# Performance work log

Hardware: AMD Instinct MI355X
Metric: run time of the kernel (lower is better)

## Reference

```python
import jax, jax.numpy as jnp
import numpy as np
from jax import lax

HD = 768; HEADS = 16; DH = HD // HEADS
KS = ((8, 8, 8), (16, 4, 4), (4, 12, 12))
ST = ((16, 32, 32), (6, 32, 32), (16, 32, 32))
T_TOK = 833; SEQ = T_TOK + 1; GH = 32


def setup_inputs() -> dict:
    key = jax.random.key(0)
    keys = iter(jax.random.split(key, 64))
    def nrm(shape, s=0.02):
        return jax.random.normal(next(keys), shape, jnp.float32) * s
    d = {}
    d["x"] = nrm((8, 3, 64, 224, 224), 1.0)
    d["spa_feas"] = nrm((8, 200, 2048), 1.0)
    d["fea_len"] = jax.random.randint(next(keys), (8,), 1, 200, dtype=jnp.int32)
    d["pos_emb"] = nrm((1, SEQ, HD), 0.02)
    d["cls_tok"] = nrm((1, 1, HD), 0.02)
    d["conv_w"] = nrm((HD, 3) + KS[0], 1.0)  # torch .normal_() std=1
    d["conv_b"] = jnp.zeros((3, HD), jnp.float32)
    d["gn_g"] = jnp.ones((HD,), jnp.float32); d["gn_b"] = jnp.zeros((HD,), jnp.float32)
    d["pin_w"] = nrm((HD, HD)); d["pin_b"] = jnp.zeros((HD,), jnp.float32)
    for nm in ("ln1", "ln2", "ln3"):
        d[nm + "_g"] = jnp.ones((HD,), jnp.float32); d[nm + "_b"] = jnp.zeros((HD,), jnp.float32)
    for nm in ("a1", "a2"):
        d[nm + "_wq"] = nrm((HD, HD)); d[nm + "_wk"] = nrm((HD, HD)); d[nm + "_wv"] = nrm((HD, HD))
        d[nm + "_wo"] = nrm((HD, HD)); d[nm + "_bo"] = jnp.zeros((HD,), jnp.float32)
    d["ff_w1"] = nrm((4 * HD, HD, 9)); d["ff_b1"] = jnp.zeros((4 * HD,), jnp.float32)
    d["ff_w2"] = nrm((HD, 4 * HD, 9)); d["ff_b2"] = jnp.zeros((HD,), jnp.float32)
    d["pout_w"] = nrm((HD, HD)); d["pout_b"] = jnp.zeros((HD,), jnp.float32)  # zero_module'd in source; random for nontrivial test
    d["spa_w"] = nrm((HD, 2048)); d["spa_b"] = jnp.zeros((HD,), jnp.float32)
    d["gru_wih"] = nrm((3 * GH, HD)); d["gru_whh"] = nrm((3 * GH, GH))
    d["gru_bih"] = jnp.zeros((3 * GH,), jnp.float32); d["gru_bhh"] = jnp.zeros((3 * GH,), jnp.float32)
    d["qh_w"] = nrm((1, GH)); d["qh_b"] = jnp.zeros((1,), jnp.float32)
    return d


def _ln(x, g, b):
    m = x.mean(-1, keepdims=True)
    v = x.var(-1, keepdims=True)
    return (x - m) / jnp.sqrt(v + 1e-5) * g + b


def _gn(x, g, b):  # x: (b, c, t), 32 groups, eps=1e-6
    bn, c, t = x.shape
    xr = x.reshape(bn, 32, c // 32, t)
    m = xr.mean((2, 3), keepdims=True)
    v = xr.var((2, 3), keepdims=True)
    xr = ((xr - m) / jnp.sqrt(v + 1e-6)).reshape(bn, c, t)
    return xr * g[None, :, None] + b[None, :, None]


def _attn(x, wq, wk, wv, wo, bo):  # self-attention, hand-rolled like source
    b, n, _ = x.shape
    q = (x @ wq.T).reshape(b, n, HEADS, DH).transpose(0, 2, 1, 3)
    k = (x @ wk.T).reshape(b, n, HEADS, DH).transpose(0, 2, 1, 3)
    v = (x @ wv.T).reshape(b, n, HEADS, DH).transpose(0, 2, 1, 3)
    sim = jnp.einsum('bhid,bhjd->bhij', q, k) * (DH ** -0.5)
    attn = jax.nn.softmax(sim, axis=-1)
    o = jnp.einsum('bhij,bhjd->bhid', attn, v).transpose(0, 2, 1, 3).reshape(b, n, HD)
    return o @ wo.T + bo


def _conv1d(x, w, b, pad):  # x: (b, c, t)
    y = lax.conv_general_dilated(x, w, (1,), [(pad, pad)],
                                 dimension_numbers=('NCH', 'OIH', 'NCH'))
    return y + b[None, :, None]


def _tokenize(x, conv_w, conv_b):
    n = x.shape[0]
    tubes = []
    for i in range(3):
        if i == 0:
            w = conv_w
        else:
            # F.interpolate(..., mode='trilinear') (align_corners=False) == jax.image.resize trilinear
            w = jax.image.resize(conv_w, (HD, 3) + KS[i], method='trilinear')
        y = lax.conv_general_dilated(x, w, ST[i], 'VALID',
                                     dimension_numbers=('NCDHW', 'OIDHW', 'NCDHW'))
        y = y + conv_b[i][None, :, None, None, None]
        tubes.append(y.reshape(n, HD, -1))
    return jnp.concatenate(tubes, -1).transpose(0, 2, 1)  # (n, 833, 768)


def _forward(x, spa_feas, fea_len, pos_emb, cls_tok, conv_w, conv_b, gn_g, gn_b,
             pin_w, pin_b, ln1_g, ln1_b, ln2_g, ln2_b, ln3_g, ln3_b,
             a1_wq, a1_wk, a1_wv, a1_wo, a1_bo, a2_wq, a2_wk, a2_wv, a2_wo, a2_bo,
             ff_w1, ff_b1, ff_w2, ff_b2, pout_w, pout_b, spa_w, spa_b,
             gru_wih, gru_whh, gru_bih, gru_bhh, qh_w, qh_b):
    tok = _tokenize(x, conv_w, conv_b)                      # (n, 833, 768)
    n = tok.shape[0]
    h = jnp.concatenate([jnp.broadcast_to(cls_tok, (n, 1, HD)), tok], 1) + pos_emb
    # TemporalEncoder (depth 1, one layer)
    hc = h.transpose(0, 2, 1)                               # (n, c, t)
    x_in = hc
    z = _gn(hc, gn_g, gn_b)
    z = jnp.einsum('oc,bct->bot', pin_w, z) + pin_b[None, :, None]  # conv1d k=1
    z = z.transpose(0, 2, 1)                                # (n, t, c)
    # BasicTransformerBlock
    z = _attn(_ln(z, ln1_g, ln1_b), a1_wq, a1_wk, a1_wv, a1_wo, a1_bo) + z
    z = _attn(_ln(z, ln2_g, ln2_b), a2_wq, a2_wk, a2_wv, a2_wo, a2_bo) + z
    f = _ln(z, ln3_g, ln3_b).transpose(0, 2, 1)
    f = _conv1d(f, ff_w1, ff_b1, 4)
    f = jax.nn.gelu(f, approximate=False)
    f = _conv1d(f, ff_w2, ff_b2, 4)
    z = f.transpose(0, 2, 1) + z
    z = z.transpose(0, 2, 1)
    z = jnp.einsum('oc,bct->bot', pout_w, z) + pout_b[None, :, None]
    h = (z + x_in).transpose(0, 2, 1)                       # (n, 834, 768)
    spa = spa_feas @ spa_w.T + spa_b                        # (n, 200, 768)
    seq = jnp.concatenate([h, spa], 1)                      # (n, 1034, 768)
    # GRU (torch cell equations), batch_first
    gx = seq @ gru_wih.T + gru_bih                          # (n, T, 3*GH)
    h0 = jnp.zeros((n, GH), seq.dtype)
    def step(hp, gx_t):
        gh = hp @ gru_whh.T + gru_bhh
        r = jax.nn.sigmoid(gx_t[:, :GH] + gh[:, :GH])
        zg = jax.nn.sigmoid(gx_t[:, GH:2 * GH] + gh[:, GH:2 * GH])
        nn_ = jnp.tanh(gx_t[:, 2 * GH:] + r * gh[:, 2 * GH:])
        hn = (1 - zg) * nn_ + zg * hp
        return hn, hn
    _, outs = lax.scan(step, h0, gx.transpose(1, 0, 2))
    outs = outs.transpose(1, 0, 2)                          # (n, T, GH)
    q = outs @ qh_w.T + qh_b                                # (n, T, 1)
    L = fea_len.astype(q.dtype) + (T_TOK + 1)
    idx = jnp.arange(q.shape[1], dtype=q.dtype)
    mask = (idx[None, :] < L[:, None]).astype(q.dtype)
    return (q[..., 0] * mask).sum(1) / L                    # per-sample masked mean


def reference(x, spa_feas, fea_len, pos_emb, cls_tok, conv_w, conv_b, gn_g, gn_b,
              pin_w, pin_b, ln1_g, ln1_b, ln2_g, ln2_b, ln3_g, ln3_b,
              a1_wq, a1_wk, a1_wv, a1_wo, a1_bo, a2_wq, a2_wk, a2_wv, a2_wo, a2_bo,
              ff_w1, ff_b1, ff_w2, ff_b2, pout_w, pout_b, spa_w, spa_b,
              gru_wih, gru_whh, gru_bih, gru_bhh, qh_w, qh_b):
    return _forward(x, spa_feas, fea_len, pos_emb, cls_tok, conv_w, conv_b, gn_g, gn_b,
                    pin_w, pin_b, ln1_g, ln1_b, ln2_g, ln2_b, ln3_g, ln3_b,
                    a1_wq, a1_wk, a1_wv, a1_wo, a1_bo, a2_wq, a2_wk, a2_wv, a2_wo, a2_bo,
                    ff_w1, ff_b1, ff_w2, ff_b2, pout_w, pout_b, spa_w, spa_b,
                    gru_wih, gru_whh, gru_bih, gru_bhh, qh_w, qh_b)
```

## Files before the change

kernel.cpp:

```cpp
#include <hip/hip_runtime.h>


typedef short bf16x8 __attribute__((ext_vector_type(8)));
typedef float f32x4 __attribute__((ext_vector_type(4)));

__device__ __forceinline__ void split_bf16(float f, ushort& h, ushort& l) {
  uint u = __float_as_uint(f);
  uint rh = (u + 0x7FFFu + ((u >> 16) & 1u)) & 0xFFFF0000u;
  h = (ushort)(rh >> 16);
  float fl = f - __uint_as_float(rh);
  uint ul = __float_as_uint(fl);
  l = (ushort)((ul + 0x7FFFu + ((ul >> 16) & 1u)) >> 16);
}

__device__ __forceinline__ ushort bf16_rnd(float f) {
  uint u = __float_as_uint(f);
  return (ushort)((u + 0x7FFFu + ((u >> 16) & 1u)) >> 16);
}

__device__ __forceinline__ float gelu_exact(float v) {
  return 0.5f * v * (1.f + erff(v * 0.70710678118654752f));
}

__global__ void wsplit_kernel(const float* __restrict__ src, ushort* __restrict__ h,
                              ushort* __restrict__ l, int n4) {
  int i = blockIdx.x * 256 + threadIdx.x;
  if (i >= n4) return;
  float4 v = *(const float4*)(src + (size_t)i * 4);
  ushort hh[4], ll[4];
  split_bf16(v.x, hh[0], ll[0]);
  split_bf16(v.y, hh[1], ll[1]);
  split_bf16(v.z, hh[2], ll[2]);
  split_bf16(v.w, hh[3], ll[3]);
  *(ushort4*)(h + (size_t)i * 4) = make_ushort4(hh[0], hh[1], hh[2], hh[3]);
  *(ushort4*)(l + (size_t)i * 4) = make_ushort4(ll[0], ll[1], ll[2], ll[3]);
}

__device__ __forceinline__ void dim_weights(int j, int O, float* w) {
  float inv = 8.0f / (float)O;
  float ks  = inv > 1.0f ? inv : 1.0f;
  float sf  = ((float)j + 0.5f) * inv - 0.5f;
  float tot = 0.f;
#pragma unroll
  for (int i = 0; i < 8; i++) {
    float xx = fabsf(sf - (float)i) / ks;
    float t  = fmaxf(0.f, 1.f - xx);
    w[i] = t; tot += t;
  }
  float r = 1.f / tot;
#pragma unroll
  for (int i = 0; i < 8; i++) w[i] *= r;
}

__global__ void resize_w_split(const float* __restrict__ src, ushort* __restrict__ dh,
                               ushort* __restrict__ dl, int OD, int OH, int OW) {
  int idx = blockIdx.x * 256 + threadIdx.x;
  int tot = 2304 * OD * OH * OW;
  if (idx >= tot) return;
  int ow = idx % OW; int t = idx / OW;
  int oh = t % OH;   t /= OH;
  int od = t % OD;   int oc = t / OD;
  float wd[8], wh[8], ww[8];
  dim_weights(od, OD, wd);
  dim_weights(oh, OH, wh);
  dim_weights(ow, OW, ww);
  const float* s = src + (size_t)oc * 512;
  float acc = 0.f;
  for (int d = 0; d < 8; d++) {
    if (wd[d] == 0.f) continue;
    for (int h = 0; h < 8; h++) {
      if (wh[h] == 0.f) continue;
      float w2 = wd[d] * wh[h];
      for (int w = 0; w < 8; w++) {
        float w3 = w2 * ww[w];
        if (w3 != 0.f) acc += w3 * s[d * 64 + h * 8 + w];
      }
    }
  }
  ushort h2, l2;
  split_bf16(acc, h2, l2);
  dh[idx] = h2; dl[idx] = l2;
}

__global__ void im2col_split(const float* __restrict__ x, ushort* __restrict__ colh,
                             ushort* __restrict__ coll, int P, int K, int L,
                             int KD, int KH, int KW, int SD, int SH, int SW) {
  int idx = blockIdx.x * 256 + threadIdx.x;
  if (idx >= P * K) return;
  int p = idx / K;  int k = idx - p * K;
  int n = p / L;    int lp = p - n * L;
  int ld = lp / 49; int r = lp - ld * 49;
  int lh = r / 7;   int lw = r - lh * 7;
  int kvol = KD * KH * KW;
  int c = k / kvol; int r2 = k - c * kvol;
  int khw = KH * KW;
  int kd = r2 / khw; int r3 = r2 - kd * khw;
  int kh = r3 / KW;  int kw = r3 - kh * KW;
  int zd = ld * SD + kd, zh = lh * SH + kh, zw = lw * SW + kw;
  float v = x[((((size_t)n * 3 + c) * 64 + zd) * 224 + zh) * 224 + zw];
  ushort h, l;
  split_bf16(v, h, l);
  colh[(size_t)p * K + k] = h;
  coll[(size_t)p * K + k] = l;
}

template <int MODE>
__global__ __launch_bounds__(256) void gemm_bf3(
    const ushort* __restrict__ Ah, const ushort* __restrict__ Al,
    const ushort* __restrict__ Bh, const ushort* __restrict__ Bl,
    int M, int N, int K,
    const float* __restrict__ bias, const float* __restrict__ res, float scale,
    float* __restrict__ of, ushort* __restrict__ oh, ushort* __restrict__ ol,
    int mapL, int mapOff, int ldo) {
  __shared__ ushort ldsA[2 * 128 * 40];
  __shared__ ushort ldsB[2 * 128 * 40];
  const int tid = threadIdx.x;
  const int wave = tid >> 6, lane = tid & 63;
  const int lrow = lane & 15, kq = lane >> 4;
  const int i0 = blockIdx.y * 128;
  const int j0 = blockIdx.x * 128;
  const int wm = (wave & 1) * 64, wn = (wave >> 1) * 64;
  const int sr = tid >> 1, sp = tid & 1;

  f32x4 acc[4][4];
#pragma unroll
  for (int mi = 0; mi < 4; mi++)
#pragma unroll
    for (int ni = 0; ni < 4; ni++) acc[mi][ni] = (f32x4)0.f;

  for (int k0 = 0; k0 < K; k0 += 32) {
    __syncthreads();
    {
      uint4 d0 = make_uint4(0, 0, 0, 0), d1 = d0, d2 = d0, d3 = d0;
      if (i0 + sr < M) {
        const ushort* s = (sp ? Al : Ah) + (size_t)(i0 + sr) * K + k0;
        d0 = *(const uint4*)(const void*)s;
        d1 = *(const uint4*)(const void*)(s + 8);
        d2 = *(const uint4*)(const void*)(s + 16);
        d3 = *(const uint4*)(const void*)(s + 24);
      }
      ushort* dst = &ldsA[sp * 5120 + sr * 40];
      *(uint4*)(void*)dst = d0; *(uint4*)(void*)(dst + 8) = d1;
      *(uint4*)(void*)(dst + 16) = d2; *(uint4*)(void*)(dst + 24) = d3;
    }
    {
      uint4 d0 = make_uint4(0, 0, 0, 0), d1 = d0, d2 = d0, d3 = d0;
      if (j0 + sr < N) {
        const ushort* s = (sp ? Bl : Bh) + (size_t)(j0 + sr) * K + k0;
        d0 = *(const uint4*)(const void*)s;
        d1 = *(const uint4*)(const void*)(s + 8);
        d2 = *(const uint4*)(const void*)(s + 16);
        d3 = *(const uint4*)(const void*)(s + 24);
      }
      ushort* dst = &ldsB[sp * 5120 + sr * 40];
      *(uint4*)(void*)dst = d0; *(uint4*)(void*)(dst + 8) = d1;
      *(uint4*)(void*)(dst + 16) = d2; *(uint4*)(void*)(dst + 24) = d3;
    }
    __syncthreads();
    bf16x8 af[2][4], bf[2][4];
#pragma unroll
    for (int p = 0; p < 2; p++)
#pragma unroll
      for (int mi = 0; mi < 4; mi++)
        af[p][mi] = *(const bf16x8*)&ldsA[p * 5120 + (wm + mi * 16 + lrow) * 40 + kq * 8];
#pragma unroll
    for (int p = 0; p < 2; p++)
#pragma unroll
      for (int ni = 0; ni < 4; ni++)
        bf[p][ni] = *(const bf16x8*)&ldsB[p * 5120 + (wn + ni * 16 + lrow) * 40 + kq * 8];
#pragma unroll
    for (int mi = 0; mi < 4; mi++)
#pragma unroll
      for (int ni = 0; ni < 4; ni++)
        acc[mi][ni] = __builtin_amdgcn_mfma_f32_16x16x32_bf16(
            af[0][mi], bf[0][ni], acc[mi][ni], 0, 0, 0);
#pragma unroll
    for (int mi = 0; mi < 4; mi++)
#pragma unroll
      for (int ni = 0; ni < 4; ni++)
        acc[mi][ni] = __builtin_amdgcn_mfma_f32_16x16x32_bf16(
            af[0][mi], bf[1][ni], acc[mi][ni], 0, 0, 0);
#pragma unroll
    for (int mi = 0; mi < 4; mi++)
#pragma unroll
      for (int ni = 0; ni < 4; ni++)
        acc[mi][ni] = __builtin_amdgcn_mfma_f32_16x16x32_bf16(
            af[1][mi], bf[0][ni], acc[mi][ni], 0, 0, 0);
  }

#pragma unroll
  for (int mi = 0; mi < 4; mi++) {
#pragma unroll
    for (int r = 0; r < 4; r++) {
      int i = i0 + wm + mi * 16 + kq * 4 + r;
      if (i >= M) continue;
#pragma unroll
      for (int ni = 0; ni < 4; ni++) {
        int j = j0 + wn + ni * 16 + lrow;
        if (j >= N) continue;
        float v = acc[mi][ni][r];
        if (MODE == 0) {
          if (bias) v += bias[j];
          of[(size_t)i * ldo + j] = v;
        } else if (MODE == 1) {
          size_t oi = (size_t)i * 768 + j;
          of[oi] = v + bias[j] + res[oi];
        } else if (MODE == 2) {
          v *= scale;
          ushort h, l;
          split_bf16(v, h, l);
          size_t oi = (size_t)i * 768 + j;
          oh[oi] = h; ol[oi] = l;
        } else {
          int nn = i / mapL; int ll = i - nn * mapL;
          size_t oi = ((size_t)(nn * 1034 + mapOff + ll)) * 768 + j;
          v += bias[j];
          if (res) v += res[oi];
          of[oi] = v;
          if (oh) {
            ushort h, l;
            split_bf16(v, h, l);
            oh[oi] = h; ol[oi] = l;
          }
        }
      }
    }
  }
}

__global__ void wprep_kernel(const float* __restrict__ W, ushort* __restrict__ wh,
                             ushort* __restrict__ wl, int J, int Cin) {
  size_t idx = (size_t)blockIdx.x * 256 + threadIdx.x;
  size_t tot = (size_t)9 * J * Cin;
  if (idx >= tot) return;
  int c = (int)(idx % Cin);
  size_t t2 = idx / Cin;
  int o = (int)(t2 % J);
  int dt = (int)(t2 / J);
  float f = W[(size_t)o * Cin * 9 + (size_t)c * 9 + dt];
  ushort h, l;
  split_bf16(f, h, l);
  wh[idx] = h; wl[idx] = l;
}

__global__ __launch_bounds__(256) void ln_split_kernel(
    const float* __restrict__ in, const float* __restrict__ g,
    const float* __restrict__ b, ushort* __restrict__ oh, ushort* __restrict__ ol) {
  int row = blockIdx.x, tid = threadIdx.x;
  int n = row / 834, t = row - n * 834;
  const float* xp = in + (size_t)row * 768;
  float v0 = xp[tid], v1 = xp[tid + 256], v2 = xp[tid + 512];
  float s = v0 + v1 + v2;
  float sq = v0 * v0 + v1 * v1 + v2 * v2;
  __shared__ float red[8];
#pragma unroll
  for (int off = 32; off >= 1; off >>= 1) {
    s += __shfl_down(s, off, 64); sq += __shfl_down(sq, off, 64);
  }
  if ((tid & 63) == 0) { red[tid >> 6] = s; red[4 + (tid >> 6)] = sq; }
  __syncthreads();
  s = red[0] + red[1] + red[2] + red[3];
  sq = red[4] + red[5] + red[6] + red[7];
  float m = s * (1.f / 768.f);
  float var = sq * (1.f / 768.f) - m * m;
  float rs = rsqrtf(var + 1e-5f);
  size_t dbase = ((size_t)(n * 842 + 4 + t)) * 768;
  ushort h, l;
  float y0 = (v0 - m) * rs * g[tid] + b[tid];
  split_bf16(y0, h, l); oh[dbase + tid] = h; ol[dbase + tid] = l;
  float y1 = (v1 - m) * rs * g[tid + 256] + b[tid + 256];
  split_bf16(y1, h, l); oh[dbase + tid + 256] = h; ol[dbase + tid + 256] = l;
  float y2 = (v2 - m) * rs * g[tid + 512] + b[tid + 512];
  split_bf16(y2, h, l); oh[dbase + tid + 512] = h; ol[dbase + tid + 512] = l;
}

__global__ void pad_zero_kernel(ushort* __restrict__ zh, ushort* __restrict__ zl,
                                ushort* __restrict__ fh, ushort* __restrict__ fl) {
  int idx = blockIdx.x * 256 + threadIdx.x;
  if (idx < 49152) {
    int c = idx % 768; int t2 = idx / 768;
    int rr = t2 & 7; int n = t2 >> 3;
    int row = (rr < 4) ? rr : (834 + rr);
    size_t d = ((size_t)(n * 842 + row)) * 768 + c;
    zh[d] = 0; zl[d] = 0;
  } else {
    int k = idx - 49152;
    if (k >= 98304) return;
    int c = k % 3072; int t2 = k / 3072;
    int rr = t2 & 7; int sl = t2 >> 3;
    int row = (rr < 4) ? rr : (834 + rr);
    size_t d = ((size_t)(sl * 842 + row)) * 3072 + c;
    fh[d] = 0; fl[d] = 0;
  }
}

template <int BN, int WM, int WN, int MODE>
__global__ __launch_bounds__(256) void conv_mfma(
    const ushort* __restrict__ Ah, const ushort* __restrict__ Al,
    const ushort* __restrict__ Wh, const ushort* __restrict__ Wl,
    int Cin, int J, int n0,
    const float* __restrict__ bias,
    ushort* __restrict__ oh, ushort* __restrict__ ol,
    float* __restrict__ of, const float* __restrict__ res) {
  const int MI = WM / 16, NI = WN / 16;
  __shared__ ushort ldsA[2 * 136 * 40];
  __shared__ ushort ldsB[2 * BN * 40];
  const int tid = threadIdx.x;
  const int wave = tid >> 6, lane = tid & 63;
  const int lrow = lane & 15, kq = lane >> 4;
  const int t0 = blockIdx.x * 128;
  const int j0 = blockIdx.y * BN;
  const int bz = blockIdx.z;
  const int n_real = n0 + bz;
  const int an = (MODE == 1) ? n_real : bz;
  const int wm = (wave & 1) * WM;
  const int wn = (wave >> 1) * WN;

  f32x4 acc[MI][NI];
#pragma unroll
  for (int mi = 0; mi < MI; mi++)
#pragma unroll
    for (int ni = 0; ni < NI; ni++) acc[mi][ni] = (f32x4)0.f;

  for (int c0 = 0; c0 < Cin; c0 += 32) {
    __syncthreads();
    for (int task = tid; task < 544; task += 256) {
      int plane = task >= 272;
      int rem = task - plane * 272;
      int r = rem >> 1, h = rem & 1;
      const ushort* src = (plane ? Al : Ah) +
          ((size_t)(an * 842 + t0 + r)) * Cin + c0 + h * 16;
      uint4 d0 = *(const uint4*)(const void*)src;
      uint4 d1 = *(const uint4*)(const void*)(src + 8);
      ushort* dst = &ldsA[plane * 5440 + r * 40 + h * 16];
      *(uint4*)(void*)dst = d0;
      *(uint4*)(void*)(dst + 8) = d1;
    }
    for (int dt = 0; dt < 9; dt++) {
      if (dt > 0) __syncthreads();
      for (int task = tid; task < 4 * BN; task += 256) {
        int plane = task >= 2 * BN;
        int rem = task - plane * 2 * BN;
        int o = rem >> 1, h = rem & 1;
        const ushort* src = (plane ? Wl : Wh) +
            ((size_t)(dt * J + j0 + o)) * Cin + c0 + h * 16;
        uint4 d0 = *(const uint4*)(const void*)src;
        uint4 d1 = *(const uint4*)(const void*)(src + 8);
        ushort* dst = &ldsB[plane * (BN * 40) + o * 40 + h * 16];
        *(uint4*)(void*)dst = d0;
        *(uint4*)(void*)(dst + 8) = d1;
      }
      __syncthreads();
      bf16x8 af[2][MI], bf[2][NI];
#pragma unroll
      for (int p = 0; p < 2; p++)
#pragma unroll
        for (int mi = 0; mi < MI; mi++)
          af[p][mi] = *(const bf16x8*)&ldsA[p * 5440 +
              (dt + wm + mi * 16 + lrow) * 40 + kq * 8];
#pragma unroll
      for (int p = 0; p < 2; p++)
#pragma unroll
        for (int ni = 0; ni < NI; ni++)
          bf[p][ni] = *(const bf16x8*)&ldsB[p * (BN * 40) +
              (wn + ni * 16 + lrow) * 40 + kq * 8];
#pragma unroll
      for (int mi = 0; mi < MI; mi++)
#pragma unroll
        for (int ni = 0; ni < NI; ni++)
          acc[mi][ni] = __builtin_amdgcn_mfma_f32_16x16x32_bf16(
              af[0][mi], bf[0][ni], acc[mi][ni], 0, 0, 0);
#pragma unroll
      for (int mi = 0; mi < MI; mi++)
#pragma unroll
        for (int ni = 0; ni < NI; ni++)
          acc[mi][ni] = __builtin_amdgcn_mfma_f32_16x16x32_bf16(
              af[0][mi], bf[1][ni], acc[mi][ni], 0, 0, 0);
#pragma unroll
      for (int mi = 0; mi < MI; mi++)
#pragma unroll
        for (int ni = 0; ni < NI; ni++)
          acc[mi][ni] = __builtin_amdgcn_mfma_f32_16x16x32_bf16(
              af[1][mi], bf[0][ni], acc[mi][ni], 0, 0, 0);
    }
  }

#pragma unroll
  for (int ni = 0; ni < NI; ni++) {
    int o = j0 + wn + ni * 16 + lrow;
    float bo = bias[o];
#pragma unroll
    for (int mi = 0; mi < MI; mi++) {
#pragma unroll
      for (int r = 0; r < 4; r++) {
        int t = t0 + wm + mi * 16 + kq * 4 + r;
        if (t < 834) {
          float v = acc[mi][ni][r] + bo;
          if (MODE == 1) {
            v = gelu_exact(v);
            ushort h, l;
            split_bf16(v, h, l);
            size_t d = ((size_t)(bz * 842 + 4 + t)) * 3072 + o;
            oh[d] = h; ol[d] = l;
          } else {
            size_t d = ((size_t)(n_real * 834 + t)) * 768 + o;
            of[d] = v + res[d];
          }
        }
      }
    }
  }
}

__global__ void addpos_kernel(float* __restrict__ seq, const float* __restrict__ pos,
                              const float* __restrict__ cls) {
  int idx = blockIdx.x * 256 + threadIdx.x;
  if (idx >= 8 * 834 * 768) return;
  int c = idx % 768;
  int t = (idx / 768) % 834;
  int n = idx / (768 * 834);
  size_t off = ((size_t)(n * 1034 + t)) * 768 + c;
  float v = (t == 0) ? cls[c] : seq[off];
  seq[off] = v + pos[(size_t)t * 768 + c];
}

__global__ __launch_bounds__(256) void groupnorm_split(
    const float* __restrict__ seq, const float* __restrict__ g,
    const float* __restrict__ b, ushort* __restrict__ oh, ushort* __restrict__ ol) {
  int blk = blockIdx.x;
  int n = blk >> 5, grp = blk & 31;
  int tid = threadIdx.x;
  float s = 0.f, sq = 0.f;
  for (int e = tid; e < 20016; e += 256) {
    int t = e / 24; int cc = e - t * 24;
    float v = seq[((size_t)(n * 1034 + t)) * 768 + grp * 24 + cc];
    s += v; sq += v * v;
  }
  __shared__ float red[8];
#pragma unroll
  for (int off = 32; off >= 1; off >>= 1) {
    s += __shfl_down(s, off, 64); sq += __shfl_down(sq, off, 64);
  }
  if ((tid & 63) == 0) { red[tid >> 6] = s; red[4 + (tid >> 6)] = sq; }
  __syncthreads();
  s = red[0] + red[1] + red[2] + red[3];
  sq = red[4] + red[5] + red[6] + red[7];
  float m = s * (1.f / 20016.f);
  float var = sq * (1.f / 20016.f) - m * m;
  float rs = rsqrtf(var + 1e-6f);
  for (int e = tid; e < 20016; e += 256) {
    int t = e / 24; int cc = e - t * 24;
    int c = grp * 24 + cc;
    float v = seq[((size_t)(n * 1034 + t)) * 768 + c];
    float y = (v - m) * rs * g[c] + b[c];
    ushort h, l;
    split_bf16(y, h, l);
    size_t d = ((size_t)(n * 834 + t)) * 768 + c;
    oh[d] = h; ol[d] = l;
  }
}

__global__ __launch_bounds__(256) void ln_rows_split(
    const float* __restrict__ in, const float* __restrict__ g,
    const float* __restrict__ b, ushort* __restrict__ oh, ushort* __restrict__ ol) {
  int row = blockIdx.x, tid = threadIdx.x;
  const float* xp = in + (size_t)row * 768;
  float v0 = xp[tid], v1 = xp[tid + 256], v2 = xp[tid + 512];
  float s = v0 + v1 + v2;
  float sq = v0 * v0 + v1 * v1 + v2 * v2;
  __shared__ float red[8];
#pragma unroll
  for (int off = 32; off >= 1; off >>= 1) {
    s += __shfl_down(s, off, 64); sq += __shfl_down(sq, off, 64);
  }
  if ((tid & 63) == 0) { red[tid >> 6] = s; red[4 + (tid >> 6)] = sq; }
  __syncthreads();
  s = red[0] + red[1] + red[2] + red[3];
  sq = red[4] + red[5] + red[6] + red[7];
  float m = s * (1.f / 768.f);
  float var = sq * (1.f / 768.f) - m * m;
  float rs = rsqrtf(var + 1e-5f);
  size_t dbase = (size_t)row * 768;
  ushort h, l;
  float y0 = (v0 - m) * rs * g[tid] + b[tid];
  split_bf16(y0, h, l); oh[dbase + tid] = h; ol[dbase + tid] = l;
  float y1 = (v1 - m) * rs * g[tid + 256] + b[tid + 256];
  split_bf16(y1, h, l); oh[dbase + tid + 256] = h; ol[dbase + tid + 256] = l;
  float y2 = (v2 - m) * rs * g[tid + 512] + b[tid + 512];
  split_bf16(y2, h, l); oh[dbase + tid + 512] = h; ol[dbase + tid + 512] = l;
}

__global__ __launch_bounds__(256) void attn_mfma(
    const ushort* __restrict__ Qh, const ushort* __restrict__ Ql,
    const ushort* __restrict__ Kh, const ushort* __restrict__ Kl,
    const ushort* __restrict__ Vh, const ushort* __restrict__ Vl,
    ushort* __restrict__ Oh, ushort* __restrict__ Ol) {
  const int S = 834;
  __shared__ ushort sm[29952];
  ushort* Qs = sm;
  ushort* Ks = sm + 9216;
  ushort* Vt = sm + 18432;
  ushort* Ps = sm + 25344;
  const int tid = threadIdx.x;
  const int wave = tid >> 6, lane = tid & 63;
  const int lrow = lane & 15, kq = lane >> 4;
  const int qt = blockIdx.x, head = blockIdx.y, n = blockIdx.z;
  const size_t base = ((size_t)n * S) * 768 + head * 48;

  for (int e = tid; e < 18432; e += 256) sm[e] = 0;
  __syncthreads();
  if (tid < 128) {
    int r = tid >> 1, p = tid & 1;
    int q = qt * 64 + r;
    if (q < S) {
      const ushort* s = (p ? Ql : Qh) + base + (size_t)q * 768;
      ushort* d = &Qs[p * 4608 + r * 72];
#pragma unroll
      for (int seg = 0; seg < 6; seg++)
        *(uint4*)(void*)(d + seg * 8) = *(const uint4*)(const void*)(s + seg * 8);
    }
  }
  __syncthreads();

  bf16x8 aq[2][2];
#pragma unroll
  for (int p = 0; p < 2; p++)
#pragma unroll
    for (int c = 0; c < 2; c++)
      aq[p][c] = *(const bf16x8*)&Qs[p * 4608 + (wave * 16 + lrow) * 72 + c * 32 + kq * 8];

  float m4[4], l4[4];
  f32x4 accO[3];
#pragma unroll
  for (int r = 0; r < 4; r++) { m4[r] = -1e30f; l4[r] = 0.f; }
#pragma unroll
  for (int d = 0; d < 3; d++) accO[d] = (f32x4)0.f;

  for (int kt = 0; kt < S; kt += 64) {
    __syncthreads();
    if (tid < 128) {
      int r = tid >> 1, p = tid & 1;
      int ki = kt + r;
      if (ki < S) {
        const ushort* s = (p ? Kl : Kh) + base + (size_t)ki * 768;
        ushort* d = &Ks[p * 4608 + r * 72];
#pragma unroll
        for (int seg = 0; seg < 6; seg++)
          *(uint4*)(void*)(d + seg * 8) = *(const uint4*)(const void*)(s + seg * 8);
      }
    }
    for (int e = tid; e < 768; e += 256) {
      int p = e >= 384;
      int rem = e - p * 384;
      int kv = rem / 6, seg = rem - kv * 6;
      if (kt + kv < S) {
        uint4 d = *(const uint4*)(const void*)((p ? Vl : Vh) + base +
                                               (size_t)(kt + kv) * 768 + seg * 8);
        ushort* dst = &Vt[p * 3456 + kv];
        uint w[4] = {d.x, d.y, d.z, d.w};
#pragma unroll
        for (int u = 0; u < 4; u++) {
          dst[(seg * 8 + u * 2 + 0) * 72] = (ushort)(w[u] & 0xFFFFu);
          dst[(seg * 8 + u * 2 + 1) * 72] = (ushort)(w[u] >> 16);
        }
      }
    }
    __syncthreads();

    f32x4 s4[4];
#pragma unroll
    for (int ni = 0; ni < 4; ni++) s4[ni] = (f32x4)0.f;
#pragma unroll
    for (int ni = 0; ni < 4; ni++) {
      bf16x8 bk[2][2];
#pragma unroll
      for (int p = 0; p < 2; p++)
#pragma unroll
        for (int c = 0; c < 2; c++)
          bk[p][c] = *(const bf16x8*)&Ks[p * 4608 + (ni * 16 + lrow) * 72 + c * 32 + kq * 8];
#pragma unroll
      for (int c = 0; c < 2; c++)
        s4[ni] = __builtin_amdgcn_mfma_f32_16x16x32_bf16(aq[0][c], bk[0][c], s4[ni], 0, 0, 0);
#pragma unroll
      for (int c = 0; c < 2; c++)
        s4[ni] = __builtin_amdgcn_mfma_f32_16x16x32_bf16(aq[0][c], bk[1][c], s4[ni], 0, 0, 0);
#pragma unroll
      for (int c = 0; c < 2; c++)
        s4[ni] = __builtin_amdgcn_mfma_f32_16x16x32_bf16(aq[1][c], bk[0][c], s4[ni], 0, 0, 0);
    }

    bool valid[4];
#pragma unroll
    for (int ni = 0; ni < 4; ni++) valid[ni] = (kt + ni * 16 + lrow) < S;
    float pv[4][4];
#pragma unroll
    for (int r = 0; r < 4; r++) {
      float sv[4], mx = -1e30f;
#pragma unroll
      for (int ni = 0; ni < 4; ni++) {
        sv[ni] = valid[ni] ? s4[ni][r] : -1e30f;
        mx = fmaxf(mx, sv[ni]);
      }
#pragma unroll
      for (int off = 8; off >= 1; off >>= 1) mx = fmaxf(mx, __shfl_xor(mx, off, 64));
      float mnew = fmaxf(m4[r], mx);
      float al = __expf(m4[r] - mnew);
      float ps = 0.f;
#pragma unroll
      for (int ni = 0; ni < 4; ni++) {
        float p = valid[ni] ? __expf(sv[ni] - mnew) : 0.f;
        pv[ni][r] = p; ps += p;
      }
#pragma unroll
      for (int off = 8; off >= 1; off >>= 1) ps += __shfl_xor(ps, off, 64);
      l4[r] = l4[r] * al + ps;
      m4[r] = mnew;
#pragma unroll
      for (int d = 0; d < 3; d++) accO[d][r] *= al;
    }
#pragma unroll
    for (int ni = 0; ni < 4; ni++)
#pragma unroll
      for (int r = 0; r < 4; r++)
        Ps[(wave * 16 + kq * 4 + r) * 72 + ni * 16 + lrow] = bf16_rnd(pv[ni][r]);

    bf16x8 ap[2];
#pragma unroll
    for (int c = 0; c < 2; c++)
      ap[c] = *(const bf16x8*)&Ps[(wave * 16 + lrow) * 72 + c * 32 + kq * 8];
#pragma unroll
    for (int d = 0; d < 3; d++) {
      bf16x8 bv[2][2];
#pragma unroll
      for (int p = 0; p < 2; p++)
#pragma unroll
        for (int c = 0; c < 2; c++)
          bv[p][c] = *(const bf16x8*)&Vt[p * 3456 + (d * 16 + lrow) * 72 + c * 32 + kq * 8];
#pragma unroll
      for (int c = 0; c < 2; c++)
        accO[d] = __builtin_amdgcn_mfma_f32_16x16x32_bf16(ap[c], bv[0][c], accO[d], 0, 0, 0);
#pragma unroll
      for (int c = 0; c < 2; c++)
        accO[d] = __builtin_amdgcn_mfma_f32_16x16x32_bf16(ap[c], bv[1][c], accO[d], 0, 0, 0);
    }
  }

#pragma unroll
  for (int r = 0; r < 4; r++) {
    int q = qt * 64 + wave * 16 + kq * 4 + r;
    if (q >= S) continue;
    float inv = 1.f / l4[r];
#pragma unroll
    for (int d = 0; d < 3; d++) {
      float v = accO[d][r] * inv;
      ushort h, l;
      split_bf16(v, h, l);
      size_t oi = base + (size_t)q * 768 + d * 16 + lrow;
      Oh[oi] = h; Ol[oi] = l;
    }
  }
}

__global__ __launch_bounds__(64) void gru_kernel(
    const float* __restrict__ gx, const float* __restrict__ whh,
    const float* __restrict__ bhh, const float* __restrict__ qh_w,
    const float* __restrict__ qh_b, const int* __restrict__ fea_len,
    float* __restrict__ out) {
  int n = blockIdx.x;
  int lane = threadIdx.x;
  bool lo = lane < 32;
  float w1[32], w2[32];
#pragma unroll
  for (int i = 0; i < 32; i++) w1[i] = whh[lane * 32 + i];
#pragma unroll
  for (int i = 0; i < 32; i++) w2[i] = lo ? whh[(64 + lane) * 32 + i] : 0.f;
  float bh1 = bhh[lane];
  float bh2 = lo ? bhh[64 + lane] : 0.f;
  float qw  = lo ? qh_w[lane] : 0.f;
  float h_all[32];
#pragma unroll
  for (int i = 0; i < 32; i++) h_all[i] = 0.f;
  float hown = 0.f, acc = 0.f;
  int L = fea_len[n] + 834;
  const float* gb = gx + (size_t)n * 1034 * 96;
  for (int t = 0; t < 1034; t++) {
    if (t >= L) break;
    const float* g = gb + (size_t)t * 96;
    float g1 = g[lane];
    float g2 = lo ? g[64 + lane] : 0.f;
    float gh1 = bh1, gh2 = bh2;
#pragma unroll
    for (int i = 0; i < 32; i++) {
      gh1 = fmaf(h_all[i], w1[i], gh1);
      gh2 = fmaf(h_all[i], w2[i], gh2);
    }
    float s1 = g1 + gh1;
    float szg = __shfl(s1, (lane + 32) & 63, 64);
    float rg = 1.f / (1.f + expf(-s1));
    float zg = 1.f / (1.f + expf(-szg));
    float nn = tanhf(fmaf(rg, gh2, g2));
    float hn = (1.f - zg) * nn + zg * hown;
    if (lo) { hown = hn; acc = fmaf(hn, qw, acc); }
#pragma unroll
    for (int i = 0; i < 32; i++) h_all[i] = __shfl(hn, i, 64);
  }
#pragma unroll
  for (int off = 16; off >= 1; off >>= 1) acc += __shfl_down(acc, off, 64);
  if (lane == 0) out[n] = acc / (float)L + qh_b[0];
}

extern "C" void kernel_launch(void* const* d_in, const int* in_sizes, int n_in,
                              void* d_out, int out_size, void* d_ws, size_t ws_size,
                              hipStream_t stream) {
  const float* x        = (const float*)d_in[0];
  const float* spa_feas = (const float*)d_in[1];
  const int*   fea_len  = (const int*)d_in[2];
  const float* pos_emb  = (const float*)d_in[3];
  const float* cls_tok  = (const float*)d_in[4];
  const float* conv_w   = (const float*)d_in[5];
  const float* conv_b   = (const float*)d_in[6];
  const float* gn_g     = (const float*)d_in[7];
  const float* gn_b     = (const float*)d_in[8];
  const float* pin_w    = (const float*)d_in[9];
  const float* pin_b    = (const float*)d_in[10];
  const float* ln_g[3]  = {(const float*)d_in[11], (const float*)d_in[13], (const float*)d_in[15]};
  const float* ln_b[3]  = {(const float*)d_in[12], (const float*)d_in[14], (const float*)d_in[16]};
  const float* wq[2] = {(const float*)d_in[17], (const float*)d_in[22]};
  const float* wk[2] = {(const float*)d_in[18], (const float*)d_in[23]};
  const float* wv[2] = {(const float*)d_in[19], (const float*)d_in[24]};
  const float* wo[2] = {(const float*)d_in[20], (const float*)d_in[25]};
  const float* bo[2] = {(const float*)d_in[21], (const float*)d_in[26]};
  const float* ff_w1 = (const float*)d_in[27];
  const float* ff_b1 = (const float*)d_in[28];
  const float* ff_w2 = (const float*)d_in[29];
  const float* ff_b2 = (const float*)d_in[30];
  const float* pout_w = (const float*)d_in[31];
  const float* pout_b = (const float*)d_in[32];
  const float* spa_w  = (const float*)d_in[33];
  const float* spa_b  = (const float*)d_in[34];
  const float* gru_wih = (const float*)d_in[35];
  const float* gru_whh = (const float*)d_in[36];
  const float* gru_bih = (const float*)d_in[37];
  const float* gru_bhh = (const float*)d_in[38];
  const float* qh_w = (const float*)d_in[39];
  const float* qh_b = (const float*)d_in[40];
  float* outp = (float*)d_out;

  float* ws  = (float*)d_ws;
  float* seq = ws;
  float* z   = seq + 6352896;
  ushort* R  = (ushort*)(ws + 11476992);

  size_t co = 0;
  ushort* pinH = R + co; co += 589824; ushort* pinL = R + co; co += 589824;
  ushort *wqH[2], *wqL[2], *wkH[2], *wkL[2], *wvH[2], *wvL[2], *woH[2], *woL[2];
  for (int l = 0; l < 2; l++) {
    wqH[l] = R + co; co += 589824; wqL[l] = R + co; co += 589824;
    wkH[l] = R + co; co += 589824; wkL[l] = R + co; co += 589824;
    wvH[l] = R + co; co += 589824; wvL[l] = R + co; co += 589824;
    woH[l] = R + co; co += 589824; woL[l] = R + co; co += 589824;
  }
  ushort* aPh = R + co; co += 5124096; ushort* aPl = R + co; co += 5124096;
  ushort* QPh = R + co; co += 5124096; ushort* QPl = R + co; co += 5124096;
  ushort* KPh = R + co; co += 5124096; ushort* KPl = R + co; co += 5124096;
  ushort* VPh = R + co; co += 5124096; ushort* VPl = R + co; co += 5124096;
  ushort* oPh = R + co; co += 5124096; ushort* oPl = R + co; co += 5124096;
  ushort* colH = R + co; co += 2709504; ushort* colL = R + co; co += 2709504;
  ushort* cwH  = R + co; co += 1179648; ushort* cwL  = R + co; co += 1179648;
  ushort* w1rH = R + co; co += 589824;  ushort* w1rL = R + co; co += 589824;
  ushort* w2rH = R + co; co += 1327104; ushort* w2rL = R + co; co += 1327104;

  ushort* zsH = R;                ushort* zsL = R + 5223936;
  ushort* fmH = R + 10447872;     ushort* fmL = R + 20997120;
  ushort* ffwH = R + 40992768;    ushort* ffwL = R + 62226432;
  ushort* zPh = R + 40992768;     ushort* zPl = R + 46116864;
  ushort* poutH = R + 51240960;   ushort* poutL = R + 51830784;
  ushort* spaWH = R + 52420608;   ushort* spaWL = R + 53993472;
  ushort* wihH = R + 55566336;    ushort* wihL = R + 55640064;
  ushort* spaInH = R + 55713792;  ushort* spaInL = R + 58990592;
  ushort* seqPh = R;              ushort* seqPl = R + 6352896;
  float* gx = (float*)(R + 12705792);

  const float QSCALE = 0.14433756729740644f;

  resize_w_split<<<2304, 256, 0, stream>>>(conv_w, w1rH, w1rL, 16, 4, 4);
  resize_w_split<<<5184, 256, 0, stream>>>(conv_w, w2rH, w2rL, 4, 12, 12);
  wsplit_kernel<<<1152, 256, 0, stream>>>(conv_w, cwH, cwL, 294912);
  im2col_split<<<9408, 256, 0, stream>>>(x, colH, colL, 1568, 1536, 196, 8, 8, 8, 16, 32, 32);
  gemm_bf3<3><<<dim3(6, 13), 256, 0, stream>>>(colH, colL, cwH, cwL, 1568, 768, 1536,
      conv_b, nullptr, 1.f, seq, nullptr, nullptr, 196, 1, 768);
  im2col_split<<<10584, 256, 0, stream>>>(x, colH, colL, 3528, 768, 441, 16, 4, 4, 6, 32, 32);
  gemm_bf3<3><<<dim3(6, 28), 256, 0, stream>>>(colH, colL, w1rH, w1rL, 3528, 768, 768,
      conv_b + 768, nullptr, 1.f, seq, nullptr, nullptr, 441, 197, 768);
  im2col_split<<<10584, 256, 0, stream>>>(x, colH, colL, 1568, 1728, 196, 4, 12, 12, 16, 32, 32);
  gemm_bf3<3><<<dim3(6, 13), 256, 0, stream>>>(colH, colL, w2rH, w2rL, 1568, 768, 1728,
      conv_b + 1536, nullptr, 1.f, seq, nullptr, nullptr, 196, 638, 768);
  addpos_kernel<<<20016, 256, 0, stream>>>(seq, pos_emb, cls_tok);

  wsplit_kernel<<<576, 256, 0, stream>>>(pin_w, pinH, pinL, 147456);
  for (int l = 0; l < 2; l++) {
    wsplit_kernel<<<576, 256, 0, stream>>>(wq[l], wqH[l], wqL[l], 147456);
    wsplit_kernel<<<576, 256, 0, stream>>>(wk[l], wkH[l], wkL[l], 147456);
    wsplit_kernel<<<576, 256, 0, stream>>>(wv[l], wvH[l], wvL[l], 147456);
    wsplit_kernel<<<576, 256, 0, stream>>>(wo[l], woH[l], woL[l], 147456);
  }

  groupnorm_split<<<256, 256, 0, stream>>>(seq, gn_g, gn_b, aPh, aPl);
  gemm_bf3<0><<<dim3(6, 53), 256, 0, stream>>>(aPh, aPl, pinH, pinL, 6672, 768, 768,
      pin_b, nullptr, 1.f, z, nullptr, nullptr, 0, 0, 768);

  for (int l = 0; l < 2; l++) {
    ln_rows_split<<<6672, 256, 0, stream>>>(z, ln_g[l], ln_b[l], aPh, aPl);
    gemm_bf3<2><<<dim3(6, 53), 256, 0, stream>>>(aPh, aPl, wqH[l], wqL[l], 6672, 768, 768,
        nullptr, nullptr, QSCALE, nullptr, QPh, QPl, 0, 0, 768);
    gemm_bf3<2><<<dim3(6, 53), 256, 0, stream>>>(aPh, aPl, wkH[l], wkL[l], 6672, 768, 768,
        nullptr, nullptr, 1.f, nullptr, KPh, KPl, 0, 0, 768);
    gemm_bf3<2><<<dim3(6, 53), 256, 0, stream>>>(aPh, aPl, wvH[l], wvL[l], 6672, 768, 768,
        nullptr, nullptr, 1.f, nullptr, VPh, VPl, 0, 0, 768);
    attn_mfma<<<dim3(14, 16, 8), 256, 0, stream>>>(QPh, QPl, KPh, KPl, VPh, VPl, oPh, oPl);
    gemm_bf3<1><<<dim3(6, 53), 256, 0, stream>>>(oPh, oPl, woH[l], woL[l], 6672, 768, 768,
        bo[l], z, 1.f, z, nullptr, nullptr, 0, 0, 768);
  }

  ln_split_kernel<<<6672, 256, 0, stream>>>(z, ln_g[2], ln_b[2], zsH, zsL);
  pad_zero_kernel<<<576, 256, 0, stream>>>(zsH, zsL, fmH, fmL);
  for (int half = 0; half < 2; half++) {
    int n0 = half * 4;
    wprep_kernel<<<82944, 256, 0, stream>>>(ff_w1, ffwH, ffwL, 3072, 768);
    conv_mfma<128, 64, 64, 1><<<dim3(7, 24, 4), 256, 0, stream>>>(
        zsH, zsL, ffwH, ffwL, 768, 3072, n0, ff_b1, fmH, fmL, nullptr, nullptr);
    wprep_kernel<<<82944, 256, 0, stream>>>(ff_w2, ffwH, ffwL, 768, 3072);
    conv_mfma<64, 64, 32, 2><<<dim3(7, 12, 4), 256, 0, stream>>>(
        fmH, fmL, ffwH, ffwL, 3072, 768, n0, ff_b2, nullptr, nullptr, z, z);
  }

  wsplit_kernel<<<5005, 256, 0, stream>>>(z, zPh, zPl, 1281024);
  wsplit_kernel<<<576, 256, 0, stream>>>(pout_w, poutH, poutL, 147456);
  wsplit_kernel<<<1536, 256, 0, stream>>>(spa_w, spaWH, spaWL, 393216);
  wsplit_kernel<<<72, 256, 0, stream>>>(gru_wih, wihH, wihL, 18432);
  wsplit_kernel<<<3200, 256, 0, stream>>>(spa_feas, spaInH, spaInL, 819200);
  gemm_bf3<3><<<dim3(6, 53), 256, 0, stream>>>(zPh, zPl, poutH, poutL, 6672, 768, 768,
      pout_b, seq, 1.f, seq, seqPh, seqPl, 834, 0, 768);
  gemm_bf3<3><<<dim3(6, 13), 256, 0, stream>>>(spaInH, spaInL, spaWH, spaWL, 1600, 768, 2048,
      spa_b, nullptr, 1.f, seq, seqPh, seqPl, 200, 834, 768);
  gemm_bf3<0><<<dim3(1, 65), 256, 0, stream>>>(seqPh, seqPl, wihH, wihL, 8272, 96, 768,
      gru_bih, nullptr, 1.f, gx, nullptr, nullptr, 0, 0, 96);
  gru_kernel<<<8, 64, 0, stream>>>(gx, gru_whh, gru_bhh, qh_w, qh_b, fea_len, outp);
}
```

Baseline: 6.222 ms.

## Restructure FFN conv to process full batch with output/K splits instead of batch halves

The feed-forward temporal conv now runs all 8 samples in one grid. The first conv is split into two output-channel halves, and the second into two K (input-channel) halves that accumulate into z, where bias is added only on the second pass. Weight prep now converts only the needed slice of weights, and the hidden buffer is enlarged to hold all 8 samples. Tile shapes change as well: the first conv uses BN 64, and the second uses a 64-row M tile over a wider grid. This raises parallelism per launch and avoids converting the full weights twice, at the cost of more memory and extra read-modify-write traffic on z.

After: 6.244 ms. No clear change (+0.4%).

```diff
diff --git a/kernel.cpp b/kernel.cpp
--- a/kernel.cpp
+++ b/kernel.cpp
@@ -229,15 +229,16 @@
 }
 
 __global__ void wprep_kernel(const float* __restrict__ W, ushort* __restrict__ wh,
-                             ushort* __restrict__ wl, int J, int Cin) {
+                             ushort* __restrict__ wl, int Jloc, int oOff,
+                             int Cloc, int cOff, int Cfull) {
   size_t idx = (size_t)blockIdx.x * 256 + threadIdx.x;
-  size_t tot = (size_t)9 * J * Cin;
+  size_t tot = (size_t)9 * Jloc * Cloc;
   if (idx >= tot) return;
-  int c = (int)(idx % Cin);
-  size_t t2 = idx / Cin;
-  int o = (int)(t2 % J);
-  int dt = (int)(t2 / J);
-  float f = W[(size_t)o * Cin * 9 + (size_t)c * 9 + dt];
+  int c = (int)(idx % Cloc);
+  size_t t2 = idx / Cloc;
+  int o = (int)(t2 % Jloc);
+  int dt = (int)(t2 / Jloc);
+  float f = W[((size_t)(oOff + o) * Cfull + (cOff + c)) * 9 + dt];
   ushort h, l;
   split_bf16(f, h, l);
   wh[idx] = h; wl[idx] = l;
@@ -274,8 +275,8 @@
   split_bf16(y2, h, l); oh[dbase + tid + 512] = h; ol[dbase + tid + 512] = l;
 }
 
-__global__ void pad_zero_kernel(ushort* __restrict__ zh, ushort* __restrict__ zl,
-                                ushort* __restrict__ fh, ushort* __restrict__ fl) {
+__global__ void pad_zero8(ushort* __restrict__ zh, ushort* __restrict__ zl,
+                          ushort* __restrict__ fh, ushort* __restrict__ fl) {
   int idx = blockIdx.x * 256 + threadIdx.x;
   if (idx < 49152) {
     int c = idx % 768; int t2 = idx / 768;
@@ -285,11 +286,11 @@
     zh[d] = 0; zl[d] = 0;
   } else {
     int k = idx - 49152;
-    if (k >= 98304) return;
+    if (k >= 196608) return;
     int c = k % 3072; int t2 = k / 3072;
-    int rr = t2 & 7; int sl = t2 >> 3;
+    int rr = t2 & 7; int n = t2 >> 3;
     int row = (rr < 4) ? rr : (834 + rr);
-    size_t d = ((size_t)(sl * 842 + row)) * 3072 + c;
+    size_t d = ((size_t)(n * 842 + row)) * 3072 + c;
     fh[d] = 0; fl[d] = 0;
   }
 }
@@ -298,21 +299,21 @@
 __global__ __launch_bounds__(256) void conv_mfma(
     const ushort* __restrict__ Ah, const ushort* __restrict__ Al,
     const ushort* __restrict__ Wh, const ushort* __restrict__ Wl,
-    int Cin, int J, int n0,
-    const float* __restrict__ bias,
+    int CinA, int cOff, int K, int J,
+    const float* __restrict__ bias, int jOff,
     ushort* __restrict__ oh, ushort* __restrict__ ol,
-    float* __restrict__ of, const float* __restrict__ res) {
-  const int MI = WM / 16, NI = WN / 16;
-  __shared__ ushort ldsA[2 * 136 * 40];
+    float* __restrict__ of) {
+  constexpr int MI = WM / 16, NI = WN / 16;
+  constexpr int BM = 2 * WM;
+  constexpr int AR = BM + 8;
+  __shared__ ushort ldsA[2 * AR * 40];
   __shared__ ushort ldsB[2 * BN * 40];
   const int tid = threadIdx.x;
   const int wave = tid >> 6, lane = tid & 63;
   const int lrow = lane & 15, kq = lane >> 4;
-  const int t0 = blockIdx.x * 128;
+  const int t0 = blockIdx.x * BM;
   const int j0 = blockIdx.y * BN;
   const int bz = blockIdx.z;
-  const int n_real = n0 + bz;
-  const int an = (MODE == 1) ? n_real : bz;
   const int wm = (wave & 1) * WM;
   const int wn = (wave >> 1) * WN;
 
@@ -322,17 +323,17 @@
 #pragma unroll
     for (int ni = 0; ni < NI; ni++) acc[mi][ni] = (f32x4)0.f;
 
-  for (int c0 = 0; c0 < Cin; c0 += 32) {
+  for (int c0 = 0; c0 < K; c0 += 32) {
     __syncthreads();
-    for (int task = tid; task < 544; task += 256) {
-      int plane = task >= 272;
-      int rem = task - plane * 272;
+    for (int task = tid; task < 4 * AR; task += 256) {
+      int plane = task >= 2 * AR;
+      int rem = task - plane * 2 * AR;
       int r = rem >> 1, h = rem & 1;
       const ushort* src = (plane ? Al : Ah) +
-          ((size_t)(an * 842 + t0 + r)) * Cin + c0 + h * 16;
+          ((size_t)(bz * 842 + t0 + r)) * CinA + cOff + c0 + h * 16;
       uint4 d0 = *(const uint4*)(const void*)src;
       uint4 d1 = *(const uint4*)(const void*)(src + 8);
-      ushort* dst = &ldsA[plane * 5440 + r * 40 + h * 16];
+      ushort* dst = &ldsA[plane * (AR * 40) + r * 40 + h * 16];
       *(uint4*)(void*)dst = d0;
       *(uint4*)(void*)(dst + 8) = d1;
     }
@@ -343,7 +344,7 @@
         int rem = task - plane * 2 * BN;
         int o = rem >> 1, h = rem & 1;
         const ushort* src = (plane ? Wl : Wh) +
-            ((size_t)(dt * J + j0 + o)) * Cin + c0 + h * 16;
+            ((size_t)(dt * J + j0 + o)) * K + c0 + h * 16;
         uint4 d0 = *(const uint4*)(const void*)src;
         uint4 d1 = *(const uint4*)(const void*)(src + 8);
         ushort* dst = &ldsB[plane * (BN * 40) + o * 40 + h * 16];
@@ -356,7 +357,7 @@
       for (int p = 0; p < 2; p++)
 #pragma unroll
         for (int mi = 0; mi < MI; mi++)
-          af[p][mi] = *(const bf16x8*)&ldsA[p * 5440 +
+          af[p][mi] = *(const bf16x8*)&ldsA[p * (AR * 40) +
               (dt + wm + mi * 16 + lrow) * 40 + kq * 8];
 #pragma unroll
       for (int p = 0; p < 2; p++)
@@ -387,8 +388,8 @@
 
 #pragma unroll
   for (int ni = 0; ni < NI; ni++) {
-    int o = j0 + wn + ni * 16 + lrow;
-    float bo = bias[o];
+    int o = jOff + j0 + wn + ni * 16 + lrow;
+    float bo = bias ? bias[o] : 0.f;
 #pragma unroll
     for (int mi = 0; mi < MI; mi++) {
 #pragma unroll
@@ -403,8 +404,8 @@
             size_t d = ((size_t)(bz * 842 + 4 + t)) * 3072 + o;
             oh[d] = h; ol[d] = l;
           } else {
-            size_t d = ((size_t)(n_real * 834 + t)) * 768 + o;
-            of[d] = v + res[d];
+            size_t d = ((size_t)(bz * 834 + t)) * 768 + o;
+            of[d] += v;
           }
         }
       }
@@ -770,9 +771,9 @@
   ushort* w1rH = R + co; co += 589824;  ushort* w1rL = R + co; co += 589824;
   ushort* w2rH = R + co; co += 1327104; ushort* w2rL = R + co; co += 1327104;
 
-  ushort* zsH = R;                ushort* zsL = R + 5223936;
-  ushort* fmH = R + 10447872;     ushort* fmL = R + 20997120;
-  ushort* ffwH = R + 40992768;    ushort* ffwL = R + 62226432;
+  ushort* fmH  = R;                ushort* fmL  = R + 20692992;
+  ushort* zsH  = R + 41385984;     ushort* zsL  = R + 46559232;
+  ushort* ffwH = R + 51732480;     ushort* ffwL = R + 62349312;
   ushort* zPh = R + 40992768;     ushort* zPl = R + 46116864;
   ushort* poutH = R + 51240960;   ushort* poutL = R + 51830784;
   ushort* spaWH = R + 52420608;   ushort* spaWL = R + 53993472;
@@ -823,15 +824,17 @@
   }
 
   ln_split_kernel<<<6672, 256, 0, stream>>>(z, ln_g[2], ln_b[2], zsH, zsL);
-  pad_zero_kernel<<<576, 256, 0, stream>>>(zsH, zsL, fmH, fmL);
-  for (int half = 0; half < 2; half++) {
-    int n0 = half * 4;
-    wprep_kernel<<<82944, 256, 0, stream>>>(ff_w1, ffwH, ffwL, 3072, 768);
-    conv_mfma<128, 64, 64, 1><<<dim3(7, 24, 4), 256, 0, stream>>>(
-        zsH, zsL, ffwH, ffwL, 768, 3072, n0, ff_b1, fmH, fmL, nullptr, nullptr);
-    wprep_kernel<<<82944, 256, 0, stream>>>(ff_w2, ffwH, ffwL, 768, 3072);
-    conv_mfma<64, 64, 32, 2><<<dim3(7, 12, 4), 256, 0, stream>>>(
-        fmH, fmL, ffwH, ffwL, 3072, 768, n0, ff_b2, nullptr, nullptr, z, z);
+  pad_zero8<<<960, 256, 0, stream>>>(zsH, zsL, fmH, fmL);
+  for (int jh = 0; jh < 2; jh++) {
+    wprep_kernel<<<41472, 256, 0, stream>>>(ff_w1, ffwH, ffwL, 1536, jh * 1536, 768, 0, 768);
+    conv_mfma<64, 64, 32, 1><<<dim3(7, 24, 8), 256, 0, stream>>>(
+        zsH, zsL, ffwH, ffwL, 768, 0, 768, 1536, ff_b1, jh * 1536, fmH, fmL, nullptr);
+  }
+  for (int kh = 0; kh < 2; kh++) {
+    wprep_kernel<<<41472, 256, 0, stream>>>(ff_w2, ffwH, ffwL, 768, 0, 1536, kh * 1536, 3072);
+    conv_mfma<64, 32, 32, 2><<<dim3(14, 12, 8), 256, 0, stream>>>(
+        fmH, fmL, ffwH, ffwL, 3072, kh * 1536, 1536, 768,
+        (kh == 1) ? ff_b2 : nullptr, 0, nullptr, nullptr, z);
   }
 
   wsplit_kernel<<<5005, 256, 0, stream>>>(z, zPh, zPl, 1281024);
```
